# Kernel optimization log

Measured on AMD Instinct MI355X. Metric: run time of the kernel, lower is better.

The kernel has to match this reference:

```python
import jax, jax.numpy as jnp
import numpy as np

EPS = 1e-6
SLIDING_WINDOW = 512
ROPE_BASE = 10000.0  # rope_local_base_freq for sliding_attention layers


def _rms_norm(x, w=None):
    # Gemma-style RMSNorm computed in fp32 then cast back
    xf = x.astype(jnp.float32)
    out = xf * jax.lax.rsqrt(jnp.mean(xf * xf, axis=-1, keepdims=True) + EPS)
    if w is not None:
        out = out * w.astype(jnp.float32)
    return out.astype(x.dtype)


def _rotate_half(x):
    x1, x2 = jnp.split(x, 2, axis=-1)
    return jnp.concatenate((-x2, x1), axis=-1)


def setup_inputs() -> dict:
    key = jax.random.key(0)
    ks = jax.random.split(key, 6)
    B, S, H, NH, NKV, D = 1, 4096, 2048, 8, 2, 256
    hidden_states = jax.random.normal(ks[0], (B, S, H), dtype=jnp.float32)
    w_q = jax.random.normal(ks[1], (H, NH * D), dtype=jnp.float32) * 0.02
    w_k = jax.random.normal(ks[2], (H, NKV * D), dtype=jnp.float32) * 0.02
    w_v = jax.random.normal(ks[3], (H, NKV * D), dtype=jnp.float32) * 0.02
    w_o = jax.random.normal(ks[4], (NH * D, H), dtype=jnp.float32) * 0.02
    q_norm_w = jnp.ones((D,), dtype=jnp.float32)
    k_norm_w = jnp.ones((D,), dtype=jnp.float32)
    # RoPE tables (local base freq, sliding layer)
    inv_freq = 1.0 / (ROPE_BASE ** (jnp.arange(0, D, 2, dtype=jnp.float32) / D))
    pos = jnp.arange(S, dtype=jnp.float32)
    freqs = pos[:, None] * inv_freq[None, :]          # [S, D/2]
    emb = jnp.concatenate((freqs, freqs), axis=-1)    # [S, D]
    cos = jnp.broadcast_to(jnp.cos(emb)[None], (B, S, D)).astype(jnp.float32)
    sin = jnp.broadcast_to(jnp.sin(emb)[None], (B, S, D)).astype(jnp.float32)
    return {"hidden_states": hidden_states, "w_q": w_q, "w_k": w_k, "w_v": w_v,
            "w_o": w_o, "q_norm_w": q_norm_w, "k_norm_w": k_norm_w,
            "cos": cos, "sin": sin}


def reference(hidden_states, w_q, w_k, w_v, w_o, q_norm_w, k_norm_w, cos, sin):
    B, S, _ = hidden_states.shape
    D = cos.shape[-1]
    NH = w_q.shape[1] // D
    NKV = w_k.shape[1] // D
    G = NH // NKV

    # projections -> [B, S, heads, D], per-head RMSNorm (Gemma3n-style)
    q = _rms_norm((hidden_states @ w_q).reshape(B, S, NH, D), q_norm_w)
    k = _rms_norm((hidden_states @ w_k).reshape(B, S, NKV, D), k_norm_w)
    v = _rms_norm((hidden_states @ w_v).reshape(B, S, NKV, D))  # v_norm: no scale

    q = q.transpose(0, 2, 1, 3)  # [B, NH, S, D]
    k = k.transpose(0, 2, 1, 3)  # [B, NKV, S, D]
    v = v.transpose(0, 2, 1, 3)

    # RoPE, cos/sin unsqueezed over the head dim
    c = cos[:, None, :, :]
    s = sin[:, None, :, :]
    q = q * c + _rotate_half(q) * s
    k = k * c + _rotate_half(k) * s

    # GQA: repeat KV heads
    k = jnp.repeat(k, G, axis=1)  # [B, NH, S, D]
    v = jnp.repeat(v, G, axis=1)

    # attention, scaling = 1.0 (q_norm replaces 1/sqrt(d) in this family)
    scores = jnp.einsum('bhqd,bhkd->bhqk', q, k)

    # causal + sliding-window mask
    i = jnp.arange(S)[:, None]
    j = jnp.arange(S)[None, :]
    mask = (j <= i) & ((i - j) < SLIDING_WINDOW)
    scores = jnp.where(mask[None, None], scores, jnp.finfo(scores.dtype).min)

    attn = jax.nn.softmax(scores.astype(jnp.float32), axis=-1).astype(q.dtype)
    out = jnp.einsum('bhqk,bhkd->bhqd', attn, v)
    out = out.transpose(0, 2, 1, 3).reshape(B, S, NH * D)
    return out @ w_o
```

## Files before the change

### kernel.cpp

```cpp
#include <hip/hip_runtime.h>
#include <hip/hip_bf16.h>

#define S_LEN 4096
#define HDIM  2048
#define NHQ   8
#define NKVH  2
#define DHEAD 256
#define WIN   512
#define NQKV  3072

typedef __hip_bfloat16 bf16_t;
using fragAB = __attribute__((ext_vector_type(8))) short;
using fragC  = __attribute__((ext_vector_type(4))) float;

typedef unsigned int u32;
typedef const __attribute__((address_space(1))) u32* gas_ptr;
typedef __attribute__((address_space(3))) u32* las_ptr;

__device__ __forceinline__ void async_copy16(const void* g, void* l) {
  __builtin_amdgcn_global_load_lds((gas_ptr)g, (las_ptr)l, 16, 0, 0);
}

#define NEG_BIG (-3.0e38f)

__device__ __forceinline__ void split2(float x, bf16_t& hi, bf16_t& lo) {
  bf16_t h = __float2bfloat16(x);
  hi = h;
  lo = __float2bfloat16(x - (float)h);
}

__global__ __launch_bounds__(256) void split_f32(
    const float* __restrict__ in, bf16_t* __restrict__ hi,
    bf16_t* __restrict__ lo, int n) {
  int i = (blockIdx.x * 256 + threadIdx.x) * 4;
  if (i >= n) return;
  float4 v = *(const float4*)(in + i);
  split2(v.x, hi[i + 0], lo[i + 0]);
  split2(v.y, hi[i + 1], lo[i + 1]);
  split2(v.z, hi[i + 2], lo[i + 2]);
  split2(v.w, hi[i + 3], lo[i + 3]);
}

__global__ __launch_bounds__(256) void transpose_cvt(
    const float* __restrict__ in, bf16_t* __restrict__ out, int R, int C) {
  __shared__ bf16_t tile[32][33];
  int c0 = blockIdx.x * 32, r0 = blockIdx.y * 32;
  int tx = threadIdx.x & 31, ty = threadIdx.x >> 5;
#pragma unroll
  for (int i = 0; i < 4; ++i)
    tile[ty + i * 8][tx] = __float2bfloat16(in[(size_t)(r0 + ty + i * 8) * C + c0 + tx]);
  __syncthreads();
#pragma unroll
  for (int i = 0; i < 4; ++i)
    out[(size_t)(c0 + ty + i * 8) * R + r0 + tx] = tile[tx][ty + i * 8];
}

__global__ __launch_bounds__(256) void transpose_split(
    const float* __restrict__ in, bf16_t* __restrict__ hiT,
    bf16_t* __restrict__ loT, int R, int C) {
  __shared__ bf16_t th[32][33];
  __shared__ bf16_t tl[32][33];
  int c0 = blockIdx.x * 32, r0 = blockIdx.y * 32;
  int tx = threadIdx.x & 31, ty = threadIdx.x >> 5;
#pragma unroll
  for (int i = 0; i < 4; ++i) {
    float x = in[(size_t)(r0 + ty + i * 8) * C + c0 + tx];
    bf16_t h, l; split2(x, h, l);
    th[ty + i * 8][tx] = h;
    tl[ty + i * 8][tx] = l;
  }
  __syncthreads();
#pragma unroll
  for (int i = 0; i < 4; ++i) {
    hiT[(size_t)(c0 + ty + i * 8) * R + r0 + tx] = th[tx][ty + i * 8];
    loT[(size_t)(c0 + ty + i * 8) * R + r0 + tx] = tl[tx][ty + i * 8];
  }
}

#define VMCNT_(n) asm volatile("s_waitcnt vmcnt(" #n ")" ::: "memory")
#define VMCNT(n) VMCNT_(n)
#define BARRIER()                     \
  {                                   \
    asm volatile("" ::: "memory");    \
    __builtin_amdgcn_s_barrier();     \
    asm volatile("" ::: "memory");    \
  }

#define MFMA_(a, b, c) __builtin_amdgcn_mfma_f32_16x16x32_bf16(a, b, c, 0, 0, 0)

#define OFF_AH 0
#define OFF_AL 16384
#define OFF_BH 32768
#define OFF_BL 45056
#define BUFSZ  57344

#define LOADB()                                                   \
  _Pragma("unroll")                                               \
  for (int j = 0; j < 3; ++j) {                                   \
    const char* bp_ = bufc + (wn + j * 16 + l16) * 64 + rdq;      \
    bh[j] = *(const fragAB*)(bp_ + OFF_BH);                       \
    bl[j] = *(const fragAB*)(bp_ + OFF_BL);                       \
  }

struct ARegs { fragAB ah0, al0, ah1, al1; };

__device__ __forceinline__ void lda_split(ARegs& r, const char* bufc, int wm,
                                          int p, int l16, int rdq) {
  const char* a0 = bufc + (wm + (2 * p) * 16 + l16) * 64 + rdq;
  const char* a1 = a0 + 16 * 64;
  r.ah0 = *(const fragAB*)(a0 + OFF_AH);
  r.al0 = *(const fragAB*)(a0 + OFF_AL);
  r.ah1 = *(const fragAB*)(a1 + OFF_AH);
  r.al1 = *(const fragAB*)(a1 + OFF_AL);
}

__device__ __forceinline__ void mfma_split(fragC (&acc)[8][3], const ARegs& r,
                                           const fragAB (&bh)[3],
                                           const fragAB (&bl)[3], int p) {
  __builtin_amdgcn_s_setprio(1);
#pragma unroll
  for (int j = 0; j < 3; ++j) {
    acc[2 * p][j]     = MFMA_(r.al0, bh[j], acc[2 * p][j]);
    acc[2 * p + 1][j] = MFMA_(r.al1, bh[j], acc[2 * p + 1][j]);
  }
#pragma unroll
  for (int j = 0; j < 3; ++j) {
    acc[2 * p][j]     = MFMA_(r.ah0, bl[j], acc[2 * p][j]);
    acc[2 * p + 1][j] = MFMA_(r.ah1, bl[j], acc[2 * p + 1][j]);
  }
#pragma unroll
  for (int j = 0; j < 3; ++j) {
    acc[2 * p][j]     = MFMA_(r.ah0, bh[j], acc[2 * p][j]);
    acc[2 * p + 1][j] = MFMA_(r.ah1, bh[j], acc[2 * p + 1][j]);
  }
  __builtin_amdgcn_s_setprio(0);
}

#define SPLIT_STEP()                        \
  {                                         \
    LOADB();                                \
    lda_split(r0, bufc, wm, 0, l16, rdq);   \
    lda_split(r1, bufc, wm, 1, l16, rdq);   \
    mfma_split(acc, r0, bh, bl, 0);         \
    lda_split(r0, bufc, wm, 2, l16, rdq);   \
    mfma_split(acc, r1, bh, bl, 1);         \
    lda_split(r1, bufc, wm, 3, l16, rdq);   \
    mfma_split(acc, r0, bh, bl, 2);         \
    mfma_split(acc, r1, bh, bl, 3);         \
  }

__global__ __launch_bounds__(512, 2) void gemm_split2(
    const bf16_t* __restrict__ Ah, const bf16_t* __restrict__ Al,
    const bf16_t* __restrict__ Bh, const bf16_t* __restrict__ Bl,
    float* __restrict__ C, int M, int N, int K) {
  __shared__ __align__(16) char lds[2 * BUFSZ];
  const int t = threadIdx.x;
  const int wave = t >> 6, lane = t & 63;
  const int quad = lane >> 4, l16 = lane & 15;
  const int m0 = blockIdx.y * 256, n0 = blockIdx.x * 192;
  const int wm = (wave >> 2) * 128, wn = (wave & 3) * 48;
  const int rdq = (quad ^ ((l16 >> 1) & 3)) * 16;

  const size_t laneOff =
      (size_t)(lane >> 2) * K * 2 + 16 * ((lane & 3) ^ ((lane >> 3) & 3));

  const char* gsrc[7];
  int ldsOff[7];
#pragma unroll
  for (int pos = 0; pos < 3; ++pos) {
    int c = wave + 8 * pos;
    if (c < 12) {
      gsrc[pos]   = (const char*)Bh + (size_t)(n0 + 16 * c) * K * 2 + laneOff;
      ldsOff[pos] = OFF_BH + c * 1024;
    } else {
      gsrc[pos]   = (const char*)Bl + (size_t)(n0 + 16 * (c - 12)) * K * 2 + laneOff;
      ldsOff[pos] = OFF_BL + (c - 12) * 1024;
    }
  }
#pragma unroll
  for (int p = 0; p < 4; ++p) {
    int sub = wave & 3;
    int R0 = ((sub >> 1) & 1) * 128 + 32 * p + (sub & 1) * 16;
    const char* base = (const char*)(wave < 4 ? Ah : Al);
    gsrc[3 + p]   = base + (size_t)(m0 + R0) * K * 2 + laneOff;
    ldsOff[3 + p] = (wave < 4 ? OFF_AH : OFF_AL) + R0 * 64;
  }

  fragC zero4 = {0.f, 0.f, 0.f, 0.f};
  fragC acc[8][3];
#pragma unroll
  for (int i = 0; i < 8; ++i)
#pragma unroll
    for (int j = 0; j < 3; ++j) acc[i][j] = zero4;

  char* ldsc = (char*)lds;
#pragma unroll
  for (int ps = 0; ps < 7; ++ps) async_copy16(gsrc[ps], ldsc + ldsOff[ps]);
#pragma unroll
  for (int ps = 0; ps < 7; ++ps) gsrc[ps] += 64;

  fragAB bh[3], bl[3];
  ARegs r0, r1;
  int cur = 0;
  const int NS = K / 32;
  for (int it = 0; it < NS - 1; ++it) {
    const char* bufc = ldsc + cur * BUFSZ;
    char* nb = ldsc + (cur ^ 1) * BUFSZ;
    VMCNT(0); BARRIER();
#pragma unroll
    for (int ps = 0; ps < 7; ++ps) async_copy16(gsrc[ps], nb + ldsOff[ps]);
#pragma unroll
    for (int ps = 0; ps < 7; ++ps) gsrc[ps] += 64;
    SPLIT_STEP();
    cur ^= 1;
  }
  {
    const char* bufc = ldsc + cur * BUFSZ;
    VMCNT(0); BARRIER();
    SPLIT_STEP();
  }

#pragma unroll
  for (int i = 0; i < 8; ++i)
#pragma unroll
    for (int j = 0; j < 3; ++j)
#pragma unroll
      for (int r = 0; r < 4; ++r) {
        int row = m0 + wm + i * 16 + quad * 4 + r;
        int col = n0 + wn + j * 16 + l16;
        C[(size_t)row * N + col] = acc[i][j][r];
      }
}

#define BT_OFF_A 0
#define BT_OFF_B 32768
#define BT_BUFSZ 49152

struct ARegs2 { fragAB a[2][2]; };

__device__ __forceinline__ void lda_bt(ARegs2& r, const char* bufc, int wm,
                                       int p, int l16, int quad, int rx) {
#pragma unroll
  for (int u = 0; u < 2; ++u)
#pragma unroll
    for (int ks = 0; ks < 2; ++ks)
      r.a[u][ks] = *(const fragAB*)(bufc + BT_OFF_A +
                                    (wm + (2 * p + u) * 16 + l16) * 128 +
                                    (((ks * 4 + quad) ^ rx) * 16));
}

__device__ __forceinline__ void mfma_bt(fragC (&acc)[8][2], const ARegs2& r,
                                        const fragAB (&b)[2][2], int p) {
  __builtin_amdgcn_s_setprio(1);
#pragma unroll
  for (int ks = 0; ks < 2; ++ks)
#pragma unroll
    for (int j = 0; j < 2; ++j) {
      acc[2 * p][j]     = MFMA_(r.a[0][ks], b[j][ks], acc[2 * p][j]);
      acc[2 * p + 1][j] = MFMA_(r.a[1][ks], b[j][ks], acc[2 * p + 1][j]);
    }
  __builtin_amdgcn_s_setprio(0);
}

#define BT_LOADB()                                                        \
  _Pragma("unroll")                                                       \
  for (int j = 0; j < 2; ++j)                                             \
  _Pragma("unroll")                                                       \
    for (int ks = 0; ks < 2; ++ks)                                        \
      bfr[j][ks] = *(const fragAB*)(bufc + BT_OFF_B +                     \
                                    (wn + j * 16 + l16) * 128 +           \
                                    (((ks * 4 + quad) ^ rx) * 16));

#define BT_STEP()                                 \
  {                                               \
    BT_LOADB();                                   \
    lda_bt(r0, bufc, wm, 0, l16, quad, rx);       \
    lda_bt(r1, bufc, wm, 1, l16, quad, rx);       \
    mfma_bt(acc, r0, bfr, 0);                     \
    lda_bt(r0, bufc, wm, 2, l16, quad, rx);       \
    mfma_bt(acc, r1, bfr, 1);                     \
    lda_bt(r1, bufc, wm, 3, l16, quad, rx);       \
    mfma_bt(acc, r0, bfr, 2);                     \
    mfma_bt(acc, r1, bfr, 3);                     \
  }

__global__ __launch_bounds__(512, 2) void gemm_bt2(
    const bf16_t* __restrict__ A, const bf16_t* __restrict__ Bt,
    float* __restrict__ C, int M, int N, int K) {
  __shared__ __align__(16) char lds[2 * BT_BUFSZ];
  const int t = threadIdx.x;
  const int wave = t >> 6, lane = t & 63;
  const int quad = lane >> 4, l16 = lane & 15;
  const int m0 = blockIdx.y * 256, n0 = blockIdx.x * 128;
  const int wm = (wave >> 2) * 128, wn = (wave & 3) * 32;
  const int rx = l16 & 7;

  const size_t laneOff =
      (size_t)(lane >> 3) * K * 2 + 16 * ((lane & 7) ^ ((lane >> 3) & 7));

  const char* gsrc[6];
  int ldsOff[6];
#pragma unroll
  for (int pos = 0; pos < 2; ++pos) {
    int c = wave + 8 * pos;
    gsrc[pos]   = (const char*)Bt + (size_t)(n0 + 8 * c) * K * 2 + laneOff;
    ldsOff[pos] = BT_OFF_B + c * 1024;
  }
#pragma unroll
  for (int p = 0; p < 4; ++p) {
    int R0 = (wave >> 2) * 128 + 32 * p + (wave & 3) * 8;
    gsrc[2 + p]   = (const char*)A + (size_t)(m0 + R0) * K * 2 + laneOff;
    ldsOff[2 + p] = BT_OFF_A + R0 * 128;
  }

  fragC zero4 = {0.f, 0.f, 0.f, 0.f};
  fragC acc[8][2];
#pragma unroll
  for (int i = 0; i < 8; ++i)
#pragma unroll
    for (int j = 0; j < 2; ++j) acc[i][j] = zero4;

  char* ldsc = (char*)lds;
#pragma unroll
  for (int ps = 0; ps < 6; ++ps) async_copy16(gsrc[ps], ldsc + ldsOff[ps]);
#pragma unroll
  for (int ps = 0; ps < 6; ++ps) gsrc[ps] += 128;

  fragAB bfr[2][2];
  ARegs2 r0, r1;
  int cur = 0;
  const int NS = K / 64;
  for (int it = 0; it < NS - 1; ++it) {
    const char* bufc = ldsc + cur * BT_BUFSZ;
    char* nb = ldsc + (cur ^ 1) * BT_BUFSZ;
    VMCNT(0); BARRIER();
#pragma unroll
    for (int ps = 0; ps < 6; ++ps) async_copy16(gsrc[ps], nb + ldsOff[ps]);
#pragma unroll
    for (int ps = 0; ps < 6; ++ps) gsrc[ps] += 128;
    BT_STEP();
    cur ^= 1;
  }
  {
    const char* bufc = ldsc + cur * BT_BUFSZ;
    VMCNT(0); BARRIER();
    BT_STEP();
  }

#pragma unroll
  for (int i = 0; i < 8; ++i)
#pragma unroll
    for (int j = 0; j < 2; ++j)
#pragma unroll
      for (int r = 0; r < 4; ++r) {
        int row = m0 + wm + i * 16 + quad * 4 + r;
        int col = n0 + wn + j * 16 + l16;
        C[(size_t)row * N + col] = acc[i][j][r];
      }
}

__global__ __launch_bounds__(256) void rmsnorm_rope_split(
    const float* __restrict__ proj, const float* __restrict__ w,
    const float* __restrict__ cosb, const float* __restrict__ sinb,
    bf16_t* __restrict__ qhi, bf16_t* __restrict__ qlo,
    int inStride, int inOff, int outStride) {
  int s = blockIdx.x, h = blockIdx.y, d = threadIdx.x;
  float x = proj[(size_t)s * inStride + inOff + h * DHEAD + d];
  float ss = x * x;
  ss += __shfl_xor(ss, 1);  ss += __shfl_xor(ss, 2);  ss += __shfl_xor(ss, 4);
  ss += __shfl_xor(ss, 8);  ss += __shfl_xor(ss, 16); ss += __shfl_xor(ss, 32);
  __shared__ float part[4];
  __shared__ float xs[DHEAD];
  if ((threadIdx.x & 63) == 0) part[threadIdx.x >> 6] = ss;
  __syncthreads();
  float tot = part[0] + part[1] + part[2] + part[3];
  float r = rsqrtf(tot * (1.0f / DHEAD) + 1e-6f);
  float xn = x * r * w[d];
  xs[d] = xn;
  __syncthreads();
  float other = xs[(d + 128) & 255];
  float rot = (d < 128) ? -other : other;
  float y = xn * cosb[(size_t)s * DHEAD + d] + rot * sinb[(size_t)s * DHEAD + d];
  bf16_t h2, l2; split2(y, h2, l2);
  size_t oidx = (size_t)s * outStride + h * DHEAD + d;
  qhi[oidx] = h2;
  qlo[oidx] = l2;
}

__global__ __launch_bounds__(256) void rmsnorm_vT(
    const float* __restrict__ proj, bf16_t* __restrict__ vt,
    int inStride, int inOff) {
  int s = blockIdx.x, h = blockIdx.y, d = threadIdx.x;
  float x = proj[(size_t)s * inStride + inOff + h * DHEAD + d];
  float ss = x * x;
  ss += __shfl_xor(ss, 1);  ss += __shfl_xor(ss, 2);  ss += __shfl_xor(ss, 4);
  ss += __shfl_xor(ss, 8);  ss += __shfl_xor(ss, 16); ss += __shfl_xor(ss, 32);
  __shared__ float part[4];
  if ((threadIdx.x & 63) == 0) part[threadIdx.x >> 6] = ss;
  __syncthreads();
  float tot = part[0] + part[1] + part[2] + part[3];
  float r = rsqrtf(tot * (1.0f / DHEAD) + 1e-6f);
  vt[((size_t)h * DHEAD + d) * S_LEN + s] = __float2bfloat16(x * r);
}

__global__ __launch_bounds__(512, 2) void attn_split(
    const bf16_t* __restrict__ Qhi, const bf16_t* __restrict__ Qlo,
    const bf16_t* __restrict__ Khi, const bf16_t* __restrict__ Klo,
    const bf16_t* __restrict__ Vt, bf16_t* __restrict__ Aout) {
  const int h = blockIdx.y;
  const int qb = blockIdx.x * 128;
  const int wave = threadIdx.x >> 6, lane = threadIdx.x & 63;
  const int quad = lane >> 4, l16 = lane & 15;
  const int qw = qb + wave * 16;
  const int kv = h >> 2;
  const bf16_t* Qh_ = Qhi + h * DHEAD;
  const bf16_t* Ql_ = Qlo + h * DHEAD;
  const bf16_t* Kh_ = Khi + kv * DHEAD;
  const bf16_t* Kl_ = Klo + kv * DHEAD;
  const bf16_t* Vh_ = Vt + (size_t)kv * DHEAD * S_LEN;

  __shared__ __align__(16) bf16_t KshH[64 * 256];
  __shared__ __align__(16) bf16_t KshL[64 * 256];
  __shared__ __align__(16) bf16_t Vsh[256 * 64];
  __shared__ __align__(16) bf16_t Plds[8][16 * 64];

  fragAB qfh[8], qfl[8];
#pragma unroll
  for (int c = 0; c < 8; ++c) {
    size_t off = (size_t)(qw + l16) * (NHQ * DHEAD) + c * 32 + quad * 8;
    qfh[c] = *(const fragAB*)(Qh_ + off);
    qfl[c] = *(const fragAB*)(Ql_ + off);
  }

  int kRow[4], kCol[4], vRow[4], vCol[4];
#pragma unroll
  for (int i = 0; i < 4; ++i) {
    int ci = i * 512 + threadIdx.x;
    kRow[i] = ci >> 5;
    kCol[i] = ((ci & 31) ^ (kRow[i] & 31)) * 8;
    vRow[i] = ci >> 3;
    vCol[i] = ((ci & 7) ^ (vRow[i] & 7)) * 8;
  }

  fragC zero4 = {0.f, 0.f, 0.f, 0.f};
  fragC o_acc[16];
#pragma unroll
  for (int c = 0; c < 16; ++c) o_acc[c] = zero4;
  float m_run[4] = {NEG_BIG, NEG_BIG, NEG_BIG, NEG_BIG};
  float l_run[4] = {0.f, 0.f, 0.f, 0.f};
  const float LOG2E = 1.4426950408889634f;

  int k_lo = qb - (WIN - 1);
  if (k_lo < 0) k_lo = 0;
  k_lo &= ~63;

  for (int kb = k_lo; kb < qb + 128; kb += 64) {
#pragma unroll
    for (int i = 0; i < 4; ++i) {
      size_t dst = (size_t)(i * 512 + threadIdx.x) * 16;
      size_t koff = (size_t)(kb + kRow[i]) * (NKVH * DHEAD) + kCol[i];
      async_copy16(Kh_ + koff, (char*)KshH + dst);
      async_copy16(Kl_ + koff, (char*)KshL + dst);
      async_copy16(Vh_ + (size_t)vRow[i] * S_LEN + kb + vCol[i], (char*)Vsh + dst);
    }
    __syncthreads();

    fragC s[4] = {zero4, zero4, zero4, zero4};
#pragma unroll
    for (int c = 0; c < 8; ++c) {
      int j = c * 4 + quad;
#pragma unroll
      for (int g = 0; g < 4; ++g) {
        int row = g * 16 + l16;
        int off = (row * 32 + (j ^ (row & 31))) * 16;
        fragAB kh = *(const fragAB*)((const char*)KshH + off);
        fragAB kl = *(const fragAB*)((const char*)KshL + off);
        s[g] = __builtin_amdgcn_mfma_f32_16x16x32_bf16(qfl[c], kh, s[g], 0, 0, 0);
        s[g] = __builtin_amdgcn_mfma_f32_16x16x32_bf16(qfh[c], kl, s[g], 0, 0, 0);
        s[g] = __builtin_amdgcn_mfma_f32_16x16x32_bf16(qfh[c], kh, s[g], 0, 0, 0);
      }
    }

    float p[4][4], alpha[4];
#pragma unroll
    for (int r = 0; r < 4; ++r) {
      int qi = qw + quad * 4 + r;
      bool vld[4];
      float sv[4];
      float mx = NEG_BIG;
#pragma unroll
      for (int g = 0; g < 4; ++g) {
        int ki = kb + g * 16 + l16;
        vld[g] = (ki <= qi) && (qi - ki < WIN);
        sv[g] = vld[g] ? s[g][r] : NEG_BIG;
        mx = fmaxf(mx, sv[g]);
      }
      mx = fmaxf(mx, __shfl_xor(mx, 1));
      mx = fmaxf(mx, __shfl_xor(mx, 2));
      mx = fmaxf(mx, __shfl_xor(mx, 4));
      mx = fmaxf(mx, __shfl_xor(mx, 8));
      float mn = fmaxf(m_run[r], mx);
      float a  = exp2f(fmaxf(m_run[r] - mn, -80.f) * LOG2E);
      float rs = 0.f;
#pragma unroll
      for (int g = 0; g < 4; ++g) {
        float e = vld[g] ? exp2f(fmaxf(s[g][r] - mn, -80.f) * LOG2E) : 0.f;
        p[g][r] = e;
        rs += e;
      }
      rs += __shfl_xor(rs, 1);
      rs += __shfl_xor(rs, 2);
      rs += __shfl_xor(rs, 4);
      rs += __shfl_xor(rs, 8);
      l_run[r] = l_run[r] * a + rs;
      m_run[r] = mn;
      alpha[r] = a;
    }
#pragma unroll
    for (int c = 0; c < 16; ++c)
#pragma unroll
      for (int r = 0; r < 4; ++r) o_acc[c][r] *= alpha[r];

    bf16_t* Pw = Plds[wave];
#pragma unroll
    for (int r = 0; r < 4; ++r)
#pragma unroll
      for (int g = 0; g < 4; ++g)
        Pw[(quad * 4 + r) * 64 + g * 16 + l16] = __float2bfloat16(p[g][r]);
    fragAB pf0 = *(const fragAB*)((const char*)Pw + l16 * 128 + quad * 16);
    fragAB pf1 = *(const fragAB*)((const char*)Pw + l16 * 128 + 64 + quad * 16);

#pragma unroll
    for (int c = 0; c < 16; ++c) {
      int d = c * 16 + l16;
#pragma unroll
      for (int ks = 0; ks < 2; ++ks) {
        int offv = (d * 8 + ((ks * 4 + quad) ^ (d & 7))) * 16;
        fragAB vf = *(const fragAB*)((const char*)Vsh + offv);
        o_acc[c] = __builtin_amdgcn_mfma_f32_16x16x32_bf16(
            ks == 0 ? pf0 : pf1, vf, o_acc[c], 0, 0, 0);
      }
    }
    __syncthreads();
  }

  float inv_l[4];
#pragma unroll
  for (int r = 0; r < 4; ++r) inv_l[r] = 1.0f / l_run[r];
#pragma unroll
  for (int c = 0; c < 16; ++c)
#pragma unroll
    for (int r = 0; r < 4; ++r) {
      int row = qw + quad * 4 + r;
      int col = h * DHEAD + c * 16 + l16;
      Aout[(size_t)row * (NHQ * DHEAD) + col] = __float2bfloat16(o_acc[c][r] * inv_l[r]);
    }
}

extern "C" void kernel_launch(void* const* d_in, const int* in_sizes, int n_in,
                              void* d_out, int out_size, void* d_ws, size_t ws_size,
                              hipStream_t stream) {
  const float* hid  = (const float*)d_in[0];
  const float* w_q  = (const float*)d_in[1];
  const float* w_k  = (const float*)d_in[2];
  const float* w_v  = (const float*)d_in[3];
  const float* w_o  = (const float*)d_in[4];
  const float* qnw  = (const float*)d_in[5];
  const float* knw  = (const float*)d_in[6];
  const float* cosb = (const float*)d_in[7];
  const float* sinb = (const float*)d_in[8];
  float* outp = (float*)d_out;

  const size_t M1 = 1048576;
  bf16_t* w = (bf16_t*)d_ws;
  bf16_t* hidh  = w;
  bf16_t* qh    = w;
  bf16_t* hidl  = w + 8 * M1;
  bf16_t* ql    = w + 8 * M1;
  bf16_t* wTh   = w + 16 * M1;
  bf16_t* kh    = w + 16 * M1;
  bf16_t* kl    = w + 18 * M1;
  bf16_t* vt    = w + 20 * M1;
  bf16_t* wTl   = w + 22 * M1;
  bf16_t* woT   = w + 22 * M1;
  float*  projqkv = (float*)(w + 28 * M1);
  bf16_t* aout  = w + 28 * M1;

  split_f32<<<(S_LEN * HDIM) / 1024, 256, 0, stream>>>(hid, hidh, hidl, S_LEN * HDIM);
  transpose_split<<<dim3((NHQ * DHEAD) / 32, HDIM / 32), 256, 0, stream>>>(
      w_q, wTh, wTl, HDIM, NHQ * DHEAD);
  transpose_split<<<dim3((NKVH * DHEAD) / 32, HDIM / 32), 256, 0, stream>>>(
      w_k, wTh + (size_t)(NHQ * DHEAD) * HDIM, wTl + (size_t)(NHQ * DHEAD) * HDIM,
      HDIM, NKVH * DHEAD);
  transpose_split<<<dim3((NKVH * DHEAD) / 32, HDIM / 32), 256, 0, stream>>>(
      w_v, wTh + (size_t)(NHQ * DHEAD + NKVH * DHEAD) * HDIM,
      wTl + (size_t)(NHQ * DHEAD + NKVH * DHEAD) * HDIM, HDIM, NKVH * DHEAD);

  gemm_split2<<<dim3(NQKV / 192, S_LEN / 256), 512, 0, stream>>>(
      hidh, hidl, wTh, wTl, projqkv, S_LEN, NQKV, HDIM);

  rmsnorm_rope_split<<<dim3(S_LEN, NHQ), 256, 0, stream>>>(
      projqkv, qnw, cosb, sinb, qh, ql, NQKV, 0, NHQ * DHEAD);
  rmsnorm_rope_split<<<dim3(S_LEN, NKVH), 256, 0, stream>>>(
      projqkv, knw, cosb, sinb, kh, kl, NQKV, NHQ * DHEAD, NKVH * DHEAD);
  rmsnorm_vT<<<dim3(S_LEN, NKVH), 256, 0, stream>>>(
      projqkv, vt, NQKV, NHQ * DHEAD + NKVH * DHEAD);

  transpose_cvt<<<dim3(HDIM / 32, (NHQ * DHEAD) / 32), 256, 0, stream>>>(w_o, woT, NHQ * DHEAD, HDIM);

  attn_split<<<dim3(S_LEN / 128, NHQ), 512, 0, stream>>>(qh, ql, kh, kl, vt, aout);

  gemm_bt2<<<dim3(HDIM / 128, S_LEN / 256), 512, 0, stream>>>(
      aout, woT, outp, S_LEN, HDIM, NHQ * DHEAD);
}
```

Measured before the change: 419.4 us.

## Double-buffer attention KV tiles, fuse transposes and norms, tile V transpose

The attention kernel now uses 32-key tiles in two LDS buffers, prefetching the next K/V tile asynchronously while the current one is computed, instead of loading a 64-key tile and synchronising before each step. The three weight transpose-split launches become one launch, and the Q and K RMSNorm+RoPE launches are merged. The V norm/transpose kernel now processes 32 rows per block through a shared tile so that the transposed writes are coalesced. Smaller key tiles mean more loop iterations and more masking and softmax overhead per key, and LDS use per block stays about the same.

New measurement: 408.7 us. 2.5% less time.

```diff
diff --git a/kernel.cpp b/kernel.cpp
--- a/kernel.cpp
+++ b/kernel.cpp
@@ -55,16 +55,22 @@
     out[(size_t)(c0 + ty + i * 8) * R + r0 + tx] = tile[tx][ty + i * 8];
 }
 
-__global__ __launch_bounds__(256) void transpose_split(
-    const float* __restrict__ in, bf16_t* __restrict__ hiT,
-    bf16_t* __restrict__ loT, int R, int C) {
+__global__ __launch_bounds__(256) void transpose_split_fused(
+    const float* __restrict__ wq, const float* __restrict__ wk,
+    const float* __restrict__ wv, bf16_t* __restrict__ hiT,
+    bf16_t* __restrict__ loT) {
   __shared__ bf16_t th[32][33];
   __shared__ bf16_t tl[32][33];
-  int c0 = blockIdx.x * 32, r0 = blockIdx.y * 32;
+  int oc = blockIdx.x * 32;
+  int r0 = blockIdx.y * 32;
+  const float* src; int C, c0;
+  if (oc < 2048)      { src = wq; C = 2048; c0 = oc; }
+  else if (oc < 2560) { src = wk; C = 512;  c0 = oc - 2048; }
+  else                { src = wv; C = 512;  c0 = oc - 2560; }
   int tx = threadIdx.x & 31, ty = threadIdx.x >> 5;
 #pragma unroll
   for (int i = 0; i < 4; ++i) {
-    float x = in[(size_t)(r0 + ty + i * 8) * C + c0 + tx];
+    float x = src[(size_t)(r0 + ty + i * 8) * C + c0 + tx];
     bf16_t h, l; split2(x, h, l);
     th[ty + i * 8][tx] = h;
     tl[ty + i * 8][tx] = l;
@@ -72,8 +78,8 @@
   __syncthreads();
 #pragma unroll
   for (int i = 0; i < 4; ++i) {
-    hiT[(size_t)(c0 + ty + i * 8) * R + r0 + tx] = th[tx][ty + i * 8];
-    loT[(size_t)(c0 + ty + i * 8) * R + r0 + tx] = tl[tx][ty + i * 8];
+    hiT[(size_t)(oc + ty + i * 8) * HDIM + r0 + tx] = th[tx][ty + i * 8];
+    loT[(size_t)(oc + ty + i * 8) * HDIM + r0 + tx] = tl[tx][ty + i * 8];
   }
 }
 
@@ -359,13 +365,23 @@
       }
 }
 
-__global__ __launch_bounds__(256) void rmsnorm_rope_split(
-    const float* __restrict__ proj, const float* __restrict__ w,
-    const float* __restrict__ cosb, const float* __restrict__ sinb,
-    bf16_t* __restrict__ qhi, bf16_t* __restrict__ qlo,
-    int inStride, int inOff, int outStride) {
-  int s = blockIdx.x, h = blockIdx.y, d = threadIdx.x;
-  float x = proj[(size_t)s * inStride + inOff + h * DHEAD + d];
+__global__ __launch_bounds__(256) void rmsnorm_rope_split_qk(
+    const float* __restrict__ proj, const float* __restrict__ qnw,
+    const float* __restrict__ knw, const float* __restrict__ cosb,
+    const float* __restrict__ sinb, bf16_t* __restrict__ qhi,
+    bf16_t* __restrict__ qlo, bf16_t* __restrict__ khi,
+    bf16_t* __restrict__ klo) {
+  int s = blockIdx.x, hb = blockIdx.y, d = threadIdx.x;
+  const float* w; bf16_t* oh; bf16_t* ol; int inOff, outStride, oBase;
+  if (hb < NHQ) {
+    w = qnw; oh = qhi; ol = qlo;
+    inOff = hb * DHEAD; outStride = NHQ * DHEAD; oBase = hb * DHEAD;
+  } else {
+    int hk = hb - NHQ;
+    w = knw; oh = khi; ol = klo;
+    inOff = NHQ * DHEAD + hk * DHEAD; outStride = NKVH * DHEAD; oBase = hk * DHEAD;
+  }
+  float x = proj[(size_t)s * NQKV + inOff + d];
   float ss = x * x;
   ss += __shfl_xor(ss, 1);  ss += __shfl_xor(ss, 2);  ss += __shfl_xor(ss, 4);
   ss += __shfl_xor(ss, 8);  ss += __shfl_xor(ss, 16); ss += __shfl_xor(ss, 32);
@@ -382,25 +398,46 @@
   float rot = (d < 128) ? -other : other;
   float y = xn * cosb[(size_t)s * DHEAD + d] + rot * sinb[(size_t)s * DHEAD + d];
   bf16_t h2, l2; split2(y, h2, l2);
-  size_t oidx = (size_t)s * outStride + h * DHEAD + d;
-  qhi[oidx] = h2;
-  qlo[oidx] = l2;
-}
-
-__global__ __launch_bounds__(256) void rmsnorm_vT(
-    const float* __restrict__ proj, bf16_t* __restrict__ vt,
-    int inStride, int inOff) {
-  int s = blockIdx.x, h = blockIdx.y, d = threadIdx.x;
-  float x = proj[(size_t)s * inStride + inOff + h * DHEAD + d];
-  float ss = x * x;
-  ss += __shfl_xor(ss, 1);  ss += __shfl_xor(ss, 2);  ss += __shfl_xor(ss, 4);
-  ss += __shfl_xor(ss, 8);  ss += __shfl_xor(ss, 16); ss += __shfl_xor(ss, 32);
-  __shared__ float part[4];
-  if ((threadIdx.x & 63) == 0) part[threadIdx.x >> 6] = ss;
+  size_t oidx = (size_t)s * outStride + oBase + d;
+  oh[oidx] = h2;
+  ol[oidx] = l2;
+}
+
+__global__ __launch_bounds__(256) void rmsnorm_vT2(
+    const float* __restrict__ proj, bf16_t* __restrict__ vt, int inOff) {
+  __shared__ float rs_[32];
+  __shared__ bf16_t tile[32][33];
+  int s0 = blockIdx.x * 32, hh = blockIdx.y;
+  const float* base = proj + (size_t)s0 * NQKV + inOff + hh * DHEAD;
+  int t = threadIdx.x;
+  int sl = t >> 3, c8 = t & 7;
+  const float4* rowp = (const float4*)(base + (size_t)sl * NQKV + c8 * 32);
+  float ss = 0.f;
+#pragma unroll
+  for (int i = 0; i < 8; ++i) {
+    float4 v = rowp[i];
+    ss += v.x * v.x + v.y * v.y + v.z * v.z + v.w * v.w;
+  }
+  ss += __shfl_xor(ss, 1); ss += __shfl_xor(ss, 2); ss += __shfl_xor(ss, 4);
+  if (c8 == 0) rs_[sl] = rsqrtf(ss * (1.0f / DHEAD) + 1e-6f);
   __syncthreads();
-  float tot = part[0] + part[1] + part[2] + part[3];
-  float r = rsqrtf(tot * (1.0f / DHEAD) + 1e-6f);
-  vt[((size_t)h * DHEAD + d) * S_LEN + s] = __float2bfloat16(x * r);
+  int tx = t & 31, ty = t >> 5;
+#pragma unroll
+  for (int ch = 0; ch < 8; ++ch) {
+#pragma unroll
+    for (int i = 0; i < 4; ++i) {
+      int s_ = ty + i * 8;
+      float x = base[(size_t)s_ * NQKV + ch * 32 + tx];
+      tile[s_][tx] = __float2bfloat16(x * rs_[s_]);
+    }
+    __syncthreads();
+#pragma unroll
+    for (int i = 0; i < 4; ++i) {
+      int dl = ty + i * 8;
+      vt[((size_t)hh * DHEAD + ch * 32 + dl) * S_LEN + s0 + tx] = tile[tx][dl];
+    }
+    __syncthreads();
+  }
 }
 
 __global__ __launch_bounds__(512, 2) void attn_split(
@@ -419,10 +456,10 @@
   const bf16_t* Kl_ = Klo + kv * DHEAD;
   const bf16_t* Vh_ = Vt + (size_t)kv * DHEAD * S_LEN;
 
-  __shared__ __align__(16) bf16_t KshH[64 * 256];
-  __shared__ __align__(16) bf16_t KshL[64 * 256];
-  __shared__ __align__(16) bf16_t Vsh[256 * 64];
-  __shared__ __align__(16) bf16_t Plds[8][16 * 64];
+  __shared__ __align__(16) bf16_t KshH[2][32 * 256];
+  __shared__ __align__(16) bf16_t KshL[2][32 * 256];
+  __shared__ __align__(16) bf16_t Vsh[2][256 * 32];
+  __shared__ __align__(16) bf16_t Plds[8][16 * 32];
 
   fragAB qfh[8], qfl[8];
 #pragma unroll
@@ -432,14 +469,25 @@
     qfl[c] = *(const fragAB*)(Ql_ + off);
   }
 
-  int kRow[4], kCol[4], vRow[4], vCol[4];
-#pragma unroll
-  for (int i = 0; i < 4; ++i) {
+  int kRow[2], kCol[2], vRow[2], vCol[2];
+#pragma unroll
+  for (int i = 0; i < 2; ++i) {
     int ci = i * 512 + threadIdx.x;
     kRow[i] = ci >> 5;
     kCol[i] = ((ci & 31) ^ (kRow[i] & 31)) * 8;
-    vRow[i] = ci >> 3;
-    vCol[i] = ((ci & 7) ^ (vRow[i] & 7)) * 8;
+    vRow[i] = ci >> 2;
+    vCol[i] = ((ci & 3) ^ (vRow[i] & 3)) * 8;
+  }
+
+#define ASTAGE(buf, kb_)                                                     \
+  _Pragma("unroll")                                                          \
+  for (int i = 0; i < 2; ++i) {                                              \
+    size_t dst = (size_t)(i * 512 + threadIdx.x) * 16;                       \
+    size_t koff = (size_t)((kb_) + kRow[i]) * (NKVH * DHEAD) + kCol[i];      \
+    async_copy16(Kh_ + koff, (char*)KshH[buf] + dst);                        \
+    async_copy16(Kl_ + koff, (char*)KshL[buf] + dst);                        \
+    async_copy16(Vh_ + (size_t)vRow[i] * S_LEN + (kb_) + vCol[i],            \
+                 (char*)Vsh[buf] + dst);                                     \
   }
 
   fragC zero4 = {0.f, 0.f, 0.f, 0.f};
@@ -452,48 +500,48 @@
 
   int k_lo = qb - (WIN - 1);
   if (k_lo < 0) k_lo = 0;
-  k_lo &= ~63;
-
-  for (int kb = k_lo; kb < qb + 128; kb += 64) {
-#pragma unroll
-    for (int i = 0; i < 4; ++i) {
-      size_t dst = (size_t)(i * 512 + threadIdx.x) * 16;
-      size_t koff = (size_t)(kb + kRow[i]) * (NKVH * DHEAD) + kCol[i];
-      async_copy16(Kh_ + koff, (char*)KshH + dst);
-      async_copy16(Kl_ + koff, (char*)KshL + dst);
-      async_copy16(Vh_ + (size_t)vRow[i] * S_LEN + kb + vCol[i], (char*)Vsh + dst);
-    }
-    __syncthreads();
-
-    fragC s[4] = {zero4, zero4, zero4, zero4};
+  k_lo &= ~31;
+
+  ASTAGE(0, k_lo);
+  int cur = 0;
+
+  for (int kb = k_lo; kb < qb + 128; kb += 32) {
+    VMCNT(0); BARRIER();
+    if (kb + 32 < qb + 128) {
+      int nbuf = cur ^ 1;
+      ASTAGE(nbuf, kb + 32);
+    }
+    const char* KH = (const char*)KshH[cur];
+    const char* KL = (const char*)KshL[cur];
+    const char* VB = (const char*)Vsh[cur];
+
+    fragC s[2] = {zero4, zero4};
 #pragma unroll
     for (int c = 0; c < 8; ++c) {
       int j = c * 4 + quad;
 #pragma unroll
-      for (int g = 0; g < 4; ++g) {
+      for (int g = 0; g < 2; ++g) {
         int row = g * 16 + l16;
         int off = (row * 32 + (j ^ (row & 31))) * 16;
-        fragAB kh = *(const fragAB*)((const char*)KshH + off);
-        fragAB kl = *(const fragAB*)((const char*)KshL + off);
+        fragAB kh = *(const fragAB*)(KH + off);
+        fragAB kl = *(const fragAB*)(KL + off);
         s[g] = __builtin_amdgcn_mfma_f32_16x16x32_bf16(qfl[c], kh, s[g], 0, 0, 0);
         s[g] = __builtin_amdgcn_mfma_f32_16x16x32_bf16(qfh[c], kl, s[g], 0, 0, 0);
         s[g] = __builtin_amdgcn_mfma_f32_16x16x32_bf16(qfh[c], kh, s[g], 0, 0, 0);
       }
     }
 
-    float p[4][4], alpha[4];
+    float p[2][4], alpha[4];
 #pragma unroll
     for (int r = 0; r < 4; ++r) {
       int qi = qw + quad * 4 + r;
-      bool vld[4];
-      float sv[4];
+      bool vld[2];
       float mx = NEG_BIG;
 #pragma unroll
-      for (int g = 0; g < 4; ++g) {
+      for (int g = 0; g < 2; ++g) {
         int ki = kb + g * 16 + l16;
         vld[g] = (ki <= qi) && (qi - ki < WIN);
-        sv[g] = vld[g] ? s[g][r] : NEG_BIG;
-        mx = fmaxf(mx, sv[g]);
+        mx = fmaxf(mx, vld[g] ? s[g][r] : NEG_BIG);
       }
       mx = fmaxf(mx, __shfl_xor(mx, 1));
       mx = fmaxf(mx, __shfl_xor(mx, 2));
@@ -503,7 +551,7 @@
       float a  = exp2f(fmaxf(m_run[r] - mn, -80.f) * LOG2E);
       float rs = 0.f;
 #pragma unroll
-      for (int g = 0; g < 4; ++g) {
+      for (int g = 0; g < 2; ++g) {
         float e = vld[g] ? exp2f(fmaxf(s[g][r] - mn, -80.f) * LOG2E) : 0.f;
         p[g][r] = e;
         rs += e;
@@ -525,23 +573,18 @@
 #pragma unroll
     for (int r = 0; r < 4; ++r)
 #pragma unroll
-      for (int g = 0; g < 4; ++g)
-        Pw[(quad * 4 + r) * 64 + g * 16 + l16] = __float2bfloat16(p[g][r]);
-    fragAB pf0 = *(const fragAB*)((const char*)Pw + l16 * 128 + quad * 16);
-    fragAB pf1 = *(const fragAB*)((const char*)Pw + l16 * 128 + 64 + quad * 16);
+      for (int g = 0; g < 2; ++g)
+        Pw[(quad * 4 + r) * 32 + g * 16 + l16] = __float2bfloat16(p[g][r]);
+    fragAB pf = *(const fragAB*)((const char*)Pw + l16 * 64 + quad * 16);
 
 #pragma unroll
     for (int c = 0; c < 16; ++c) {
       int d = c * 16 + l16;
-#pragma unroll
-      for (int ks = 0; ks < 2; ++ks) {
-        int offv = (d * 8 + ((ks * 4 + quad) ^ (d & 7))) * 16;
-        fragAB vf = *(const fragAB*)((const char*)Vsh + offv);
-        o_acc[c] = __builtin_amdgcn_mfma_f32_16x16x32_bf16(
-            ks == 0 ? pf0 : pf1, vf, o_acc[c], 0, 0, 0);
-      }
-    }
-    __syncthreads();
+      int offv = (d * 4 + (quad ^ (d & 3))) * 16;
+      fragAB vf = *(const fragAB*)(VB + offv);
+      o_acc[c] = __builtin_amdgcn_mfma_f32_16x16x32_bf16(pf, vf, o_acc[c], 0, 0, 0);
+    }
+    cur ^= 1;
   }
 
   float inv_l[4];
@@ -555,6 +598,7 @@
       int col = h * DHEAD + c * 16 + l16;
       Aout[(size_t)row * (NHQ * DHEAD) + col] = __float2bfloat16(o_acc[c][r] * inv_l[r]);
     }
+#undef ASTAGE
 }
 
 extern "C" void kernel_launch(void* const* d_in, const int* in_sizes, int n_in,
@@ -587,24 +631,16 @@
   bf16_t* aout  = w + 28 * M1;
 
   split_f32<<<(S_LEN * HDIM) / 1024, 256, 0, stream>>>(hid, hidh, hidl, S_LEN * HDIM);
-  transpose_split<<<dim3((NHQ * DHEAD) / 32, HDIM / 32), 256, 0, stream>>>(
-      w_q, wTh, wTl, HDIM, NHQ * DHEAD);
-  transpose_split<<<dim3((NKVH * DHEAD) / 32, HDIM / 32), 256, 0, stream>>>(
-      w_k, wTh + (size_t)(NHQ * DHEAD) * HDIM, wTl + (size_t)(NHQ * DHEAD) * HDIM,
-      HDIM, NKVH * DHEAD);
-  transpose_split<<<dim3((NKVH * DHEAD) / 32, HDIM / 32), 256, 0, stream>>>(
-      w_v, wTh + (size_t)(NHQ * DHEAD + NKVH * DHEAD) * HDIM,
-      wTl + (size_t)(NHQ * DHEAD + NKVH * DHEAD) * HDIM, HDIM, NKVH * DHEAD);
+  transpose_split_fused<<<dim3(NQKV / 32, HDIM / 32), 256, 0, stream>>>(
+      w_q, w_k, w_v, wTh, wTl);
 
   gemm_split2<<<dim3(NQKV / 192, S_LEN / 256), 512, 0, stream>>>(
       hidh, hidl, wTh, wTl, projqkv, S_LEN, NQKV, HDIM);
 
-  rmsnorm_rope_split<<<dim3(S_LEN, NHQ), 256, 0, stream>>>(
-      projqkv, qnw, cosb, sinb, qh, ql, NQKV, 0, NHQ * DHEAD);
-  rmsnorm_rope_split<<<dim3(S_LEN, NKVH), 256, 0, stream>>>(
-      projqkv, knw, cosb, sinb, kh, kl, NQKV, NHQ * DHEAD, NKVH * DHEAD);
-  rmsnorm_vT<<<dim3(S_LEN, NKVH), 256, 0, stream>>>(
-      projqkv, vt, NQKV, NHQ * DHEAD + NKVH * DHEAD);
+  rmsnorm_rope_split_qk<<<dim3(S_LEN, NHQ + NKVH), 256, 0, stream>>>(
+      projqkv, qnw, knw, cosb, sinb, qh, ql, kh, kl);
+  rmsnorm_vT2<<<dim3(S_LEN / 32, NKVH), 256, 0, stream>>>(
+      projqkv, vt, NHQ * DHEAD + NKVH * DHEAD);
 
   transpose_cvt<<<dim3(HDIM / 32, (NHQ * DHEAD) / 32), 256, 0, stream>>>(w_o, woT, NHQ * DHEAD, HDIM);
 
```
